# Kernel optimization log

Hardware: AMD Instinct MI355X
Metric: run time of the kernel (lower is better)

Reference implementation:

```python
import math
import jax, jax.numpy as jnp
import numpy as np

N = 2048          # batch size
D = 256           # embedding_dim
MEM = 16384       # memory_size
ANOMALY_WEIGHT = 1.0
TEMP = 0.1
MOMENTUM = 0.01
NCLS = 2          # binary phishing labels -> max(labels.max()+1, 2) == 2


def setup_inputs() -> dict:
    key = jax.random.key(0)
    ks = jax.random.split(key, 10)
    s = 1.0 / math.sqrt(D)  # nn.Linear default init range
    return {
        'z': jax.random.normal(ks[0], (N, D), jnp.float32),
        'labels': jax.random.randint(ks[1], (N,), 0, NCLS),
        'memory': jax.random.normal(ks[2], (MEM, D), jnp.float32),
        'memory_weights': jax.random.uniform(ks[3], (MEM,), jnp.float32),
        'running_mean': jnp.zeros((D,), jnp.float32),
        'running_cov': jnp.eye(D, dtype=jnp.float32),
        'Wq': jax.random.uniform(ks[4], (D, D), jnp.float32, -s, s),
        'bq': jax.random.uniform(ks[5], (D,), jnp.float32, -s, s),
        'Wk': jax.random.uniform(ks[6], (D, D), jnp.float32, -s, s),
        'bk': jax.random.uniform(ks[7], (D,), jnp.float32, -s, s),
        'Wv': jax.random.uniform(ks[8], (D, D), jnp.float32, -s, s),
        'bv': jax.random.uniform(ks[9], (D,), jnp.float32, -s, s),
    }


def reference(z, labels, memory, memory_weights, running_mean, running_cov,
              Wq, bq, Wk, bk, Wv, bv):
    # ---- update(z.detach(), labels): entire update path is detached in torch ----
    z_sg = jax.lax.stop_gradient(z)

    # _update_stats: EMA of batch mean / covariance (done before importance)
    mu = z_sg.mean(axis=0)                                  # [D]
    zc = z_sg - mu
    cov = zc.T @ zc / max(N - 1, 1)                         # [D, D]
    rm = (1.0 - MOMENTUM) * running_mean + MOMENTUM * mu
    rc = (1.0 - MOMENTUM) * running_cov + MOMENTUM * cov

    # _mahalanobis with updated running stats
    c = z_sg - rm
    cov_inv = jnp.linalg.inv(rc + 1e-6 * jnp.eye(D, dtype=rc.dtype))
    dist = jnp.sqrt(jnp.clip(jnp.einsum('nd,de,ne->n', c, cov_inv, c), 1e-8))
    a_norm = (dist - dist.min()) / (dist.max() - dist.min() + 1e-8)

    # _mi_proxy: KL(batch label dist || uniform), broadcast to all items
    counts = jnp.zeros((NCLS,), z.dtype).at[labels].add(1.0)
    p = counts / jnp.clip(counts.sum(), 1.0)
    # p / uniform == p * NCLS; clip inside log for safety (both classes present)
    kl = jnp.clip((p * jnp.log(jnp.clip(p * NCLS, 1e-8))).sum(), 0.0)
    importance = (1.0 + ANOMALY_WEIGHT * a_norm) * kl       # [N]

    # serial top-1 priority-queue eviction, in descending-importance order
    order = jnp.argsort(-importance)
    z_ord = z_sg[order]
    imp_ord = importance[order]

    def evict_step(state, inp):
        mem, w = state
        zi, imp = inp
        j = jnp.argmin(w)                   # weakest memory slot
        rep = imp > w[j]
        mem = mem.at[j].set(jnp.where(rep, zi, mem[j]))
        w = w.at[j].set(jnp.where(rep, imp, w[j]))
        return (mem, w), None

    (mem, _), _ = jax.lax.scan(evict_step, (memory, memory_weights), (z_ord, imp_ord))

    # ---- query(z): cross-attention over the (full) updated memory ----
    Q = z @ Wq.T + bq                       # [N, D]
    K = mem @ Wk.T + bk                     # [MEM, D]
    V = mem @ Wv.T + bv                     # [MEM, D]
    sc = (Q @ K.T) / math.sqrt(D)           # [N, MEM]
    attn = jax.nn.softmax(sc / TEMP, axis=-1)
    return z + 0.5 * (attn @ V)
```

## Files before the change

### kernel.cpp

```cpp
#include <hip/hip_runtime.h>
#include <math.h>

#define NB   2048
#define DE   256
#define MEMN 16384
#define CAND_CAP 256
#define FSPL 16
#define FKPS 1024
#define FIT  32

typedef __attribute__((ext_vector_type(8)))  short  short8;
typedef __attribute__((ext_vector_type(16))) float  float16;

static const size_t OFF_QB   = 0;
static const size_t OFF_KB   = 262144;
static const size_t OFF_VTB  = 2359296;
static const size_t OFF_LP   = 4456448;
static const size_t OFF_OPB  = 4521984;
static const size_t SO_A    = 0;
static const size_t SO_X    = 65536;
static const size_t SO_MUP  = 131072;
static const size_t SO_DIST = 147456;

__device__ inline unsigned short f2bf(float f) {
  unsigned u = __float_as_uint(f);
  unsigned r = (u + 0x7fffu + ((u >> 16) & 1u)) >> 16;
  return (unsigned short)r;
}
__device__ inline float bf2f(unsigned short s) {
  return __uint_as_float((unsigned)s << 16);
}

__device__ inline void bitonic_sort_u64(unsigned long long* key, int n, int tid, int nth) {
  for (int k = 2; k <= n; k <<= 1) {
    for (int j = k >> 1; j > 0; j >>= 1) {
      __syncthreads();
      for (int i = tid; i < n; i += nth) {
        int ixj = i ^ j;
        if (ixj > i) {
          unsigned long long a = key[i], b = key[ixj];
          bool up = ((i & k) == 0);
          if ((a > b) == up) { key[i] = b; key[ixj] = a; }
        }
      }
    }
  }
  __syncthreads();
}

__global__ __launch_bounds__(256) void mupart_kernel(const float* __restrict__ z,
                                                     float* __restrict__ mup,
                                                     float* __restrict__ Az) {
  int d = threadIdx.x;
  int r0 = blockIdx.x * 32;
  float4 zero4 = {0.f, 0.f, 0.f, 0.f};
  *(float4*)&Az[(size_t)blockIdx.x * 1024 + threadIdx.x * 4] = zero4;
  float s = 0.f;
  for (int r = 0; r < 32; ++r) s += z[(size_t)(r0 + r) * DE + d];
  mup[blockIdx.x * DE + d] = s;
}

__global__ __launch_bounds__(256) void covpart_kernel(const float* __restrict__ z,
                                                      float* __restrict__ A) {
  __shared__ float As[16][68];
  __shared__ float Bs[16][68];
  int tid = threadIdx.x, tx = tid & 15, ty = tid >> 4;
  int i0 = blockIdx.x * 64, j0 = blockIdx.y * 64;
  int nbase = blockIdx.z * 128;
  float acc[4][4] = {};
  for (int nt = 0; nt < 8; ++nt) {
    int n0 = nbase + nt * 16;
    for (int e = tid; e < 1024; e += 256) {
      int c = e & 63, nn = e >> 6;
      As[nn][c] = z[(size_t)(n0 + nn) * DE + i0 + c];
      Bs[nn][c] = z[(size_t)(n0 + nn) * DE + j0 + c];
    }
    __syncthreads();
#pragma unroll
    for (int nn = 0; nn < 16; ++nn) {
      float4 a4 = *(const float4*)&As[nn][ty * 4];
      float4 b4 = *(const float4*)&Bs[nn][tx * 4];
      acc[0][0] += a4.x*b4.x; acc[0][1] += a4.x*b4.y; acc[0][2] += a4.x*b4.z; acc[0][3] += a4.x*b4.w;
      acc[1][0] += a4.y*b4.x; acc[1][1] += a4.y*b4.y; acc[1][2] += a4.y*b4.z; acc[1][3] += a4.y*b4.w;
      acc[2][0] += a4.z*b4.x; acc[2][1] += a4.z*b4.y; acc[2][2] += a4.z*b4.z; acc[2][3] += a4.z*b4.w;
      acc[3][0] += a4.w*b4.x; acc[3][1] += a4.w*b4.y; acc[3][2] += a4.w*b4.z; acc[3][3] += a4.w*b4.w;
    }
    __syncthreads();
  }
  for (int r = 0; r < 4; ++r) {
    int i = i0 + ty * 4 + r;
    for (int c = 0; c < 4; ++c) {
      int j = j0 + tx * 4 + c;
      atomicAdd(&A[(size_t)i * DE + j], acc[r][c]);
    }
  }
}

__global__ __launch_bounds__(256) void gemmx_kernel(const float* __restrict__ ZtZ,
                                                    const float* __restrict__ rcov,
                                                    const float* __restrict__ mup,
                                                    float* __restrict__ X) {
  __shared__ float Ea[16][17];
  __shared__ float Eb[16][17];
  __shared__ float mus[256];
  int t = threadIdx.x, tx = t & 15, ty = t >> 4;
  int i0 = blockIdx.x * 16, j0 = blockIdx.y * 16;
  {
    float s = 0.f;
    for (int b = 0; b < 64; ++b) s += mup[b * DE + t];
    mus[t] = s;
  }
  __syncthreads();
  const float c1 = 0.01f / (float)(NB - 1);
  const float invN = 1.0f / (float)NB;
  float acc = 0.f;
  for (int k0 = 0; k0 < 256; k0 += 16) {
    int c = k0 + tx;
    {
      int r = i0 + ty;
      float base = 0.99f * rcov[(size_t)r * DE + c] +
                   c1 * (ZtZ[(size_t)r * DE + c] - mus[r] * mus[c] * invN);
      float e = -base;
      if (r == c) e += 1.0f - 1e-6f;
      Ea[ty][tx] = e;
    }
    {
      int r = j0 + ty;
      float base = 0.99f * rcov[(size_t)r * DE + c] +
                   c1 * (ZtZ[(size_t)r * DE + c] - mus[r] * mus[c] * invN);
      float e = -base;
      if (r == c) e += 1.0f - 1e-6f;
      Eb[ty][tx] = e;
    }
    __syncthreads();
#pragma unroll
    for (int k = 0; k < 16; ++k) acc += Ea[ty][k] * Eb[tx][k];
    __syncthreads();
  }
  int r = i0 + ty, c = j0 + tx;
  float base = 0.99f * rcov[(size_t)r * DE + c] +
               c1 * (ZtZ[(size_t)r * DE + c] - mus[r] * mus[c] * invN);
  float e = -base;
  if (r == c) e += 1.0f - 1e-6f;
  X[(size_t)r * DE + c] = acc + e + ((r == c) ? 1.0f : 0.0f);
}

__global__ __launch_bounds__(256) void dist_kernel(const float* __restrict__ z,
                                                   const float* __restrict__ rmean,
                                                   const float* __restrict__ mup,
                                                   const float* __restrict__ X,
                                                   float* __restrict__ dist) {
  __shared__ float cc[4][256];
  __shared__ float4 red[256];
  int n0 = blockIdx.x * 4, i = threadIdx.x;
  float s = 0.f;
  for (int b = 0; b < 64; ++b) s += mup[b * DE + i];
  float rmi = 0.99f * rmean[i] + 0.01f * s * (1.0f / (float)NB);
#pragma unroll
  for (int r = 0; r < 4; ++r) cc[r][i] = z[(size_t)(n0 + r) * DE + i] - rmi;
  __syncthreads();
  float y0 = 0.f, y1 = 0.f, y2 = 0.f, y3 = 0.f;
#pragma unroll 8
  for (int j = 0; j < DE; ++j) {
    float x = X[(size_t)j * DE + i];
    y0 += x * cc[0][j]; y1 += x * cc[1][j]; y2 += x * cc[2][j]; y3 += x * cc[3][j];
  }
  float4 v;
  v.x = y0 * cc[0][i]; v.y = y1 * cc[1][i]; v.z = y2 * cc[2][i]; v.w = y3 * cc[3][i];
  red[i] = v;
  __syncthreads();
  for (int sH = 128; sH > 0; sH >>= 1) {
    if (i < sH) {
      float4 a = red[i], b = red[i + sH];
      a.x += b.x; a.y += b.y; a.z += b.z; a.w += b.w;
      red[i] = a;
    }
    __syncthreads();
  }
  if (i < 4) {
    float4 tt = red[0];
    float d = (i == 0) ? tt.x : (i == 1) ? tt.y : (i == 2) ? tt.z : tt.w;
    dist[n0 + i] = sqrtf(fmaxf(d, 1e-8f));
  }
}

__global__ __launch_bounds__(1024) void update_kernel(const float* __restrict__ dist,
                                                      const int* __restrict__ labels,
                                                      const float* __restrict__ weights,
                                                      const float* __restrict__ z,
                                                      float* __restrict__ memory) {
  __shared__ unsigned long long ikeys[NB];
  __shared__ unsigned long long ck[CAND_CAP];
  __shared__ unsigned long long mred[1024];
  __shared__ int slots[CAND_CAP], srcs[CAND_CAP];
  __shared__ float smin[1024], smax[1024];
  __shared__ int scnt[1024];
  __shared__ float s_kl, s_dmin, s_inv;
  __shared__ int s_ccnt, s_m, s_stop;
  int t = threadIdx.x;

  float mn = 1e30f, mx = -1e30f; int c1 = 0;
  for (int n = t; n < NB; n += 1024) {
    float d = dist[n];
    mn = fminf(mn, d); mx = fmaxf(mx, d);
    c1 += labels[n];
  }
  smin[t] = mn; smax[t] = mx; scnt[t] = c1;
  __syncthreads();
  for (int s = 512; s > 0; s >>= 1) {
    if (t < s) {
      smin[t] = fminf(smin[t], smin[t + s]);
      smax[t] = fmaxf(smax[t], smax[t + s]);
      scnt[t] += scnt[t + s];
    }
    __syncthreads();
  }
  if (t == 0) {
    float p1 = (float)scnt[0] / (float)NB;
    float p0 = (float)(NB - scnt[0]) / (float)NB;
    float kl = p0 * logf(fmaxf(2.f * p0, 1e-8f)) + p1 * logf(fmaxf(2.f * p1, 1e-8f));
    s_kl = fmaxf(kl, 0.f);
    s_dmin = smin[0];
    s_inv = 1.0f / (smax[0] - smin[0] + 1e-8f);
    s_ccnt = 0; s_m = 0; s_stop = 0;
  }
  __syncthreads();
  float kl = s_kl;

  for (int n = t; n < NB; n += 1024) {
    float imp = (1.0f + (dist[n] - s_dmin) * s_inv) * kl;
    ikeys[n] = ((unsigned long long)(unsigned)(~__float_as_uint(imp)) << 32) | (unsigned)n;
  }
  float thresh = 2.f * kl;
  for (int j = t; j < MEMN; j += 1024) {
    float wv = weights[j];
    if (wv < thresh) {
      int p = atomicAdd(&s_ccnt, 1);
      if (p < CAND_CAP) ck[p] = ((unsigned long long)__float_as_uint(wv) << 32) | (unsigned)j;
    }
  }
  __syncthreads();
  int C = s_ccnt; if (C > CAND_CAP) C = CAND_CAP;
  for (int i = t; i < CAND_CAP; i += 1024)
    if (i >= C) ck[i] = 0xFFFFFFFFFFFFFFFFULL;
  bitonic_sort_u64(ck, CAND_CAP, t, 1024);

  float prevv = 0.f;
  for (int i = 0; i < C; ++i) {
    unsigned long long mymin = ikeys[t] < ikeys[t + 1024] ? ikeys[t] : ikeys[t + 1024];
    mred[t] = mymin;
    __syncthreads();
    for (int s = 512; s > 0; s >>= 1) {
      if (t < s) { if (mred[t + s] < mred[t]) mred[t] = mred[t + s]; }
      __syncthreads();
    }
    if (t == 0) {
      unsigned long long best = mred[0];
      float im = __uint_as_float(~(unsigned)(best >> 32));
      float wv = __uint_as_float((unsigned)(ck[i] >> 32));
      bool ok = (im > wv) && (i == 0 || prevv >= wv);
      if (ok) {
        slots[s_m] = (int)(ck[i] & 0xffffffffULL);
        srcs[s_m]  = (int)(best & 0xffffffffULL);
        s_m++;
        prevv = im;
        ikeys[(int)(best & 0xffffffffULL)] = ~0ULL;
      } else {
        s_stop = 1;
      }
    }
    __syncthreads();
    if (s_stop) break;
  }
  int m = s_m;
  for (int e = t; e < m * DE; e += 1024) {
    int i = e >> 8, d = e & 255;
    memory[(size_t)slots[i] * DE + d] = z[(size_t)srcs[i] * DE + d];
  }
}

__global__ __launch_bounds__(256, 1) void qkv_kernel(
    const float* __restrict__ z, const float* __restrict__ memory,
    const float* __restrict__ Wq, const float* __restrict__ bq,
    const float* __restrict__ Wk, const float* __restrict__ bk,
    const float* __restrict__ Wv, const float* __restrict__ bv,
    unsigned short* __restrict__ Qbf, unsigned short* __restrict__ Kbf,
    unsigned short* __restrict__ Vtb) {
  __shared__ unsigned short Bsh[64 * 264];
  int flat = blockIdx.x;
  const float *Af, *Bf, *bias;
  unsigned short* C;
  int bias_row, vtile, gx, gy, ldC;
  if (flat < 64) {
    gx = flat & 15; gy = flat >> 4;
    Af = z; Bf = Wq; bias = bq; bias_row = 0; vtile = 0; C = Qbf; ldC = DE;
  } else if (flat < 576) {
    int f = flat - 64; gx = f & 127; gy = f >> 7;
    Af = memory; Bf = Wk; bias = bk; bias_row = 0; vtile = 0; C = Kbf; ldC = DE;
  } else {
    int f = flat - 576; gx = f & 1; gy = f >> 1;
    Af = Wv; Bf = memory; bias = bv; bias_row = 1; vtile = 1; C = Vtb; ldC = 0;
  }

  int tid = threadIdx.x;
  int w = tid >> 6, lane = tid & 63;
  int m = lane & 31, h = lane >> 5;
  int arow = gx * 128 + w * 32 + m;
  int n0 = gy * 64;

  short8 af[16];
#pragma unroll
  for (int kc = 0; kc < 16; ++kc) {
    const float* src = &Af[(size_t)arow * DE + kc * 16 + h * 8];
    float4 f0 = *(const float4*)&src[0];
    float4 f1 = *(const float4*)&src[4];
    short8 v;
    v[0] = (short)f2bf(f0.x); v[1] = (short)f2bf(f0.y);
    v[2] = (short)f2bf(f0.z); v[3] = (short)f2bf(f0.w);
    v[4] = (short)f2bf(f1.x); v[5] = (short)f2bf(f1.y);
    v[6] = (short)f2bf(f1.z); v[7] = (short)f2bf(f1.w);
    af[kc] = v;
  }
  {
    int r = tid >> 2, q = tid & 3;
    const float* src = &Bf[(size_t)(n0 + r) * DE + q * 64];
    unsigned short* dst = &Bsh[r * 264 + q * 64];
#pragma unroll
    for (int j = 0; j < 8; ++j) {
      float4 f0 = *(const float4*)&src[j * 8];
      float4 f1 = *(const float4*)&src[j * 8 + 4];
      short8 v;
      v[0] = (short)f2bf(f0.x); v[1] = (short)f2bf(f0.y);
      v[2] = (short)f2bf(f0.z); v[3] = (short)f2bf(f0.w);
      v[4] = (short)f2bf(f1.x); v[5] = (short)f2bf(f1.y);
      v[6] = (short)f2bf(f1.z); v[7] = (short)f2bf(f1.w);
      *(short8*)&dst[j * 8] = v;
    }
  }
  __syncthreads();

  float16 a0 = {}, a1 = {};
#pragma unroll
  for (int kc = 0; kc < 16; ++kc) {
    short8 b0 = *(const short8*)&Bsh[(0 * 32 + m) * 264 + kc * 16 + h * 8];
    short8 b1 = *(const short8*)&Bsh[(1 * 32 + m) * 264 + kc * 16 + h * 8];
    a0 = __builtin_amdgcn_mfma_f32_32x32x16_bf16(af[kc], b0, a0, 0, 0, 0);
    a1 = __builtin_amdgcn_mfma_f32_32x32x16_bf16(af[kc], b1, a1, 0, 0, 0);
  }
#pragma unroll
  for (int r = 0; r < 16; ++r) {
    int rr = (r & 3) + 8 * (r >> 2) + 4 * h;
    int orow = gx * 128 + w * 32 + rr;
    int oc0 = n0 + m, oc1 = n0 + 32 + m;
    float bb0 = bias_row ? bias[orow] : bias[oc0];
    float bb1 = bias_row ? bias[orow] : bias[oc1];
    if (!vtile) {
      C[(size_t)orow * ldC + oc0] = f2bf(a0[r] + bb0);
      C[(size_t)orow * ldC + oc1] = f2bf(a1[r] + bb1);
    } else {
      C[(size_t)(oc0 >> 5) * 8192 + (size_t)orow * 32 + (oc0 & 31)] = f2bf(a0[r] + bb0);
      C[(size_t)(oc1 >> 5) * 8192 + (size_t)orow * 32 + (oc1 & 31)] = f2bf(a1[r] + bb1);
    }
  }
}

__global__ __launch_bounds__(256, 2) void flash_kernel(
    const unsigned short* __restrict__ Qb, const unsigned short* __restrict__ Kb,
    const unsigned short* __restrict__ Vtb, unsigned short* __restrict__ Opb,
    float* __restrict__ Lp) {
  __shared__ unsigned short Ks[32 * 264];
  __shared__ unsigned short Vs[128 * 40];
  __shared__ unsigned short Ps[4][32 * 40];

  int tid = threadIdx.x;
  int w = tid >> 6, lane = tid & 63;
  int m = lane & 31, h = lane >> 5;
  int sp = blockIdx.x, qg = blockIdx.y, dh = blockIdx.z;
  int myrow = qg * 128 + w * 32 + m;

  short8 qf[16];
#pragma unroll
  for (int kc = 0; kc < 16; ++kc)
    qf[kc] = *(const short8*)&Qb[(size_t)myrow * DE + kc * 16 + h * 8];
  short8 ones;
#pragma unroll
  for (int j = 0; j < 8; ++j) ones[j] = (short)0x3F80;

  float16 O[4] = {};
  float16 l = {};

  short8 kreg[4], vreg[2];
  {
    int kb = sp * FKPS;
#pragma unroll
    for (int i = 0; i < 4; ++i) {
      int c = i * 256 + tid, kr = c >> 5, kc = c & 31;
      kreg[i] = *(const short8*)&Kb[(size_t)(kb + kr) * DE + kc * 8];
    }
    const unsigned short* vg = &Vtb[(size_t)(kb >> 5) * 8192 + (size_t)dh * 4096];
#pragma unroll
    for (int i = 0; i < 2; ++i) {
      int c = i * 256 + tid;
      vreg[i] = *(const short8*)&vg[c * 8];
    }
  }

  for (int it = 0; it < FIT; ++it) {
    __syncthreads();
#pragma unroll
    for (int i = 0; i < 4; ++i) {
      int c = i * 256 + tid, kr = c >> 5, kc = c & 31;
      *(short8*)&Ks[kr * 264 + kc * 8] = kreg[i];
    }
#pragma unroll
    for (int i = 0; i < 2; ++i) {
      int c = i * 256 + tid, dr = c >> 2, dc = c & 3;
      *(short8*)&Vs[dr * 40 + dc * 8] = vreg[i];
    }
    if (it + 1 < FIT) {
      int kb = sp * FKPS + (it + 1) * 32;
#pragma unroll
      for (int i = 0; i < 4; ++i) {
        int c = i * 256 + tid, kr = c >> 5, kc = c & 31;
        kreg[i] = *(const short8*)&Kb[(size_t)(kb + kr) * DE + kc * 8];
      }
      const unsigned short* vg = &Vtb[(size_t)(kb >> 5) * 8192 + (size_t)dh * 4096];
#pragma unroll
      for (int i = 0; i < 2; ++i) {
        int c = i * 256 + tid;
        vreg[i] = *(const short8*)&vg[c * 8];
      }
    }
    __syncthreads();

    float16 s0 = {}, s1 = {};
    __builtin_amdgcn_s_setprio(1);
#pragma unroll
    for (int kc = 0; kc < 16; kc += 2) {
      short8 b0 = *(const short8*)&Ks[m * 264 + kc * 16 + h * 8];
      short8 b1 = *(const short8*)&Ks[m * 264 + (kc + 1) * 16 + h * 8];
      s0 = __builtin_amdgcn_mfma_f32_32x32x16_bf16(qf[kc], b0, s0, 0, 0, 0);
      s1 = __builtin_amdgcn_mfma_f32_32x32x16_bf16(qf[kc + 1], b1, s1, 0, 0, 0);
    }
    __builtin_amdgcn_s_setprio(0);
#pragma unroll
    for (int r = 0; r < 16; ++r) {
      int row = (r & 3) + 8 * (r >> 2) + 4 * h;
      Ps[w][row * 40 + m] = f2bf(__expf(fmaf(s0[r] + s1[r], 0.625f, -11.0903549f)));
    }
    short8 pa0 = *(const short8*)&Ps[w][m * 40 + h * 8];
    short8 pa1 = *(const short8*)&Ps[w][m * 40 + 16 + h * 8];
    __builtin_amdgcn_s_setprio(1);
    l = __builtin_amdgcn_mfma_f32_32x32x16_bf16(pa0, ones, l, 0, 0, 0);
    l = __builtin_amdgcn_mfma_f32_32x32x16_bf16(pa1, ones, l, 0, 0, 0);
#pragma unroll
    for (int ct = 0; ct < 4; ++ct) {
      short8 vb0 = *(const short8*)&Vs[(ct * 32 + m) * 40 + h * 8];
      short8 vb1 = *(const short8*)&Vs[(ct * 32 + m) * 40 + 16 + h * 8];
      O[ct] = __builtin_amdgcn_mfma_f32_32x32x16_bf16(pa0, vb0, O[ct], 0, 0, 0);
      O[ct] = __builtin_amdgcn_mfma_f32_32x32x16_bf16(pa1, vb1, O[ct], 0, 0, 0);
    }
    __builtin_amdgcn_s_setprio(0);
  }

  size_t ob = ((size_t)sp * NB + qg * 128 + w * 32) * DE + dh * 128;
#pragma unroll
  for (int ct = 0; ct < 4; ++ct)
#pragma unroll
    for (int r = 0; r < 16; ++r) {
      int rr = (r & 3) + 8 * (r >> 2) + 4 * h;
      Opb[ob + (size_t)rr * DE + ct * 32 + m] = f2bf(O[ct][r]);
    }
  if (dh == 0 && m == 0) {
#pragma unroll
    for (int r = 0; r < 16; ++r) {
      int rr = (r & 3) + 8 * (r >> 2) + 4 * h;
      Lp[sp * NB + qg * 128 + w * 32 + rr] = l[r];
    }
  }
}

__global__ __launch_bounds__(256) void combine_kernel(const float* __restrict__ z,
                                                      const unsigned short* __restrict__ Opb,
                                                      const float* __restrict__ Lp,
                                                      float* __restrict__ out) {
  int n = blockIdx.x, c = threadIdx.x;
  float num = 0.f, den = 0.f;
#pragma unroll
  for (int s = 0; s < FSPL; ++s) {
    den += Lp[s * NB + n];
    num += bf2f(Opb[((size_t)s * NB + n) * DE + c]);
  }
  size_t base = (size_t)n * DE + c;
  out[base] = z[base] + 0.5f * num / den;
}

extern "C" void kernel_launch(void* const* d_in, const int* in_sizes, int n_in,
                              void* d_out, int out_size, void* d_ws, size_t ws_size,
                              hipStream_t stream) {
  (void)in_sizes; (void)n_in; (void)out_size; (void)ws_size;
  const float* z       = (const float*)d_in[0];
  const int*   labels  = (const int*)d_in[1];
  float*       memory  = (float*)d_in[2];
  const float* weights = (const float*)d_in[3];
  const float* rmean   = (const float*)d_in[4];
  const float* rcov    = (const float*)d_in[5];
  const float* Wq      = (const float*)d_in[6];
  const float* bq      = (const float*)d_in[7];
  const float* Wk      = (const float*)d_in[8];
  const float* bk      = (const float*)d_in[9];
  const float* Wv      = (const float*)d_in[10];
  const float* bv      = (const float*)d_in[11];
  float* out = (float*)d_out;
  float* ws  = (float*)d_ws;

  unsigned short* Qbf = (unsigned short*)(ws + OFF_QB);
  unsigned short* Kbf = (unsigned short*)(ws + OFF_KB);
  unsigned short* Vtb = (unsigned short*)(ws + OFF_VTB);
  float* Lp           = ws + OFF_LP;
  unsigned short* Opb = (unsigned short*)(ws + OFF_OPB);
  float* SB    = ws + OFF_OPB;
  float* A     = SB + SO_A;
  float* X     = SB + SO_X;
  float* mup   = SB + SO_MUP;
  float* dist  = SB + SO_DIST;

  mupart_kernel<<<64, 256, 0, stream>>>(z, mup, A);
  covpart_kernel<<<dim3(4, 4, 16), 256, 0, stream>>>(z, A);
  gemmx_kernel<<<dim3(16, 16), 256, 0, stream>>>(A, rcov, mup, X);
  dist_kernel<<<NB / 4, 256, 0, stream>>>(z, rmean, mup, X, dist);
  update_kernel<<<1, 1024, 0, stream>>>(dist, labels, weights, z, memory);
  qkv_kernel<<<1088, 256, 0, stream>>>(z, memory, Wq, bq, Wk, bk, Wv, bv, Qbf, Kbf, Vtb);
  flash_kernel<<<dim3(FSPL, NB / 128, 2), 256, 0, stream>>>(Qbf, Kbf, Vtb, Opb, Lp);
  combine_kernel<<<NB, 256, 0, stream>>>(z, Opb, Lp, out);
}
```

Baseline: 259.1 us.

## Double-buffer K/V LDS tiles in flash kernel with one barrier per iteration

The flash attention loop now keeps two LDS buffers for the K and V tiles. It stores the next tile into the alternate buffer while computing on the current one, which cuts the two barriers per iteration down to one and overlaps the LDS writes with the MFMA work. The exponential is also rewritten as exp2f with pre-scaled constants. The cost is doubled LDS use for K and V, which could lower occupancy, and a slightly different rounding of the softmax numerator.

```diff
diff --git a/kernel.cpp b/kernel.cpp
--- a/kernel.cpp
+++ b/kernel.cpp
@@ -368,8 +368,8 @@
     const unsigned short* __restrict__ Qb, const unsigned short* __restrict__ Kb,
     const unsigned short* __restrict__ Vtb, unsigned short* __restrict__ Opb,
     float* __restrict__ Lp) {
-  __shared__ unsigned short Ks[32 * 264];
-  __shared__ unsigned short Vs[128 * 40];
+  __shared__ unsigned short Ks[2][32 * 264];
+  __shared__ unsigned short Vs[2][128 * 40];
   __shared__ unsigned short Ps[4][32 * 40];
 
   int tid = threadIdx.x;
@@ -389,56 +389,53 @@
   float16 O[4] = {};
   float16 l = {};
 
+  int kc_r = tid >> 5, kc_c = tid & 31;
+  int vd_r = tid >> 2, vd_c = tid & 3;
+
   short8 kreg[4], vreg[2];
-  {
-    int kb = sp * FKPS;
-#pragma unroll
-    for (int i = 0; i < 4; ++i) {
-      int c = i * 256 + tid, kr = c >> 5, kc = c & 31;
-      kreg[i] = *(const short8*)&Kb[(size_t)(kb + kr) * DE + kc * 8];
-    }
-    const unsigned short* vg = &Vtb[(size_t)(kb >> 5) * 8192 + (size_t)dh * 4096];
-#pragma unroll
-    for (int i = 0; i < 2; ++i) {
-      int c = i * 256 + tid;
-      vreg[i] = *(const short8*)&vg[c * 8];
-    }
-  }
+#define LOAD_TILE(kb_)                                                          \
+  {                                                                             \
+    int kb = (kb_);                                                             \
+    _Pragma("unroll")                                                           \
+    for (int i = 0; i < 4; ++i) {                                               \
+      int c = i * 256 + tid, kr = c >> 5, kcol = c & 31;                        \
+      kreg[i] = *(const short8*)&Kb[(size_t)(kb + kr) * DE + kcol * 8];         \
+    }                                                                           \
+    const unsigned short* vg = &Vtb[(size_t)((kb) >> 5) * 8192 + (size_t)dh * 4096]; \
+    _Pragma("unroll")                                                           \
+    for (int i = 0; i < 2; ++i) {                                               \
+      int c = i * 256 + tid;                                                    \
+      vreg[i] = *(const short8*)&vg[c * 8];                                     \
+    }                                                                           \
+  }
+#define STORE_TILE(buf)                                                         \
+  {                                                                             \
+    _Pragma("unroll")                                                           \
+    for (int i = 0; i < 4; ++i)                                                 \
+      *(short8*)&Ks[buf][(kc_r + i * 8) * 264 + kc_c * 8] = kreg[i];            \
+    _Pragma("unroll")                                                           \
+    for (int i = 0; i < 2; ++i)                                                 \
+      *(short8*)&Vs[buf][(vd_r + i * 64) * 40 + vd_c * 8] = vreg[i];            \
+  }
+
+  LOAD_TILE(sp * FKPS);
+  STORE_TILE(0);
+  LOAD_TILE(sp * FKPS + 32);
+  __syncthreads();
 
   for (int it = 0; it < FIT; ++it) {
-    __syncthreads();
-#pragma unroll
-    for (int i = 0; i < 4; ++i) {
-      int c = i * 256 + tid, kr = c >> 5, kc = c & 31;
-      *(short8*)&Ks[kr * 264 + kc * 8] = kreg[i];
-    }
-#pragma unroll
-    for (int i = 0; i < 2; ++i) {
-      int c = i * 256 + tid, dr = c >> 2, dc = c & 3;
-      *(short8*)&Vs[dr * 40 + dc * 8] = vreg[i];
-    }
+    int cur = it & 1;
     if (it + 1 < FIT) {
-      int kb = sp * FKPS + (it + 1) * 32;
-#pragma unroll
-      for (int i = 0; i < 4; ++i) {
-        int c = i * 256 + tid, kr = c >> 5, kc = c & 31;
-        kreg[i] = *(const short8*)&Kb[(size_t)(kb + kr) * DE + kc * 8];
-      }
-      const unsigned short* vg = &Vtb[(size_t)(kb >> 5) * 8192 + (size_t)dh * 4096];
-#pragma unroll
-      for (int i = 0; i < 2; ++i) {
-        int c = i * 256 + tid;
-        vreg[i] = *(const short8*)&vg[c * 8];
-      }
-    }
-    __syncthreads();
+      STORE_TILE(cur ^ 1);
+      if (it + 2 < FIT) LOAD_TILE(sp * FKPS + (it + 2) * 32);
+    }
 
     float16 s0 = {}, s1 = {};
     __builtin_amdgcn_s_setprio(1);
 #pragma unroll
     for (int kc = 0; kc < 16; kc += 2) {
-      short8 b0 = *(const short8*)&Ks[m * 264 + kc * 16 + h * 8];
-      short8 b1 = *(const short8*)&Ks[m * 264 + (kc + 1) * 16 + h * 8];
+      short8 b0 = *(const short8*)&Ks[cur][m * 264 + kc * 16 + h * 8];
+      short8 b1 = *(const short8*)&Ks[cur][m * 264 + (kc + 1) * 16 + h * 8];
       s0 = __builtin_amdgcn_mfma_f32_32x32x16_bf16(qf[kc], b0, s0, 0, 0, 0);
       s1 = __builtin_amdgcn_mfma_f32_32x32x16_bf16(qf[kc + 1], b1, s1, 0, 0, 0);
     }
@@ -446,7 +443,7 @@
 #pragma unroll
     for (int r = 0; r < 16; ++r) {
       int row = (r & 3) + 8 * (r >> 2) + 4 * h;
-      Ps[w][row * 40 + m] = f2bf(__expf(fmaf(s0[r] + s1[r], 0.625f, -11.0903549f)));
+      Ps[w][row * 40 + m] = f2bf(exp2f(fmaf(s0[r] + s1[r], 0.90168440f, -16.0f)));
     }
     short8 pa0 = *(const short8*)&Ps[w][m * 40 + h * 8];
     short8 pa1 = *(const short8*)&Ps[w][m * 40 + 16 + h * 8];
@@ -455,13 +452,16 @@
     l = __builtin_amdgcn_mfma_f32_32x32x16_bf16(pa1, ones, l, 0, 0, 0);
 #pragma unroll
     for (int ct = 0; ct < 4; ++ct) {
-      short8 vb0 = *(const short8*)&Vs[(ct * 32 + m) * 40 + h * 8];
-      short8 vb1 = *(const short8*)&Vs[(ct * 32 + m) * 40 + 16 + h * 8];
+      short8 vb0 = *(const short8*)&Vs[cur][(ct * 32 + m) * 40 + h * 8];
+      short8 vb1 = *(const short8*)&Vs[cur][(ct * 32 + m) * 40 + 16 + h * 8];
       O[ct] = __builtin_amdgcn_mfma_f32_32x32x16_bf16(pa0, vb0, O[ct], 0, 0, 0);
       O[ct] = __builtin_amdgcn_mfma_f32_32x32x16_bf16(pa1, vb1, O[ct], 0, 0, 0);
     }
     __builtin_amdgcn_s_setprio(0);
-  }
+    __syncthreads();
+  }
+#undef LOAD_TILE
+#undef STORE_TILE
 
   size_t ob = ((size_t)sp * NB + qg * 128 + w * 32) * DE + dh * 128;
 #pragma unroll
```

Measured after the change: 263.2 us. No clear change (+1.6%).

## Keep softmax probabilities in registers via transposed QK MFMA and lane swaps

Applied to the files above, without the earlier changes.

Swaps the MFMA operands so the score tile comes out transposed, letting each lane hold one query row's probabilities. These are packed to bf16 with v_cvt_pk_bf16_f32 and exchanged across half-waves with permlane32_swap, so they can feed the PV MFMA directly without the LDS staging buffer. The row sum is now accumulated in scalar registers instead of through an MFMA against a vector of ones, and the exponent uses exp2f with the scale folded into the constant. The point is to cut LDS writes, LDS reads, a barrier-like dependency and two MFMAs per iteration. The cost is more VALU work and reliance on the lane layout being right.

```diff
diff --git a/kernel.cpp b/kernel.cpp
--- a/kernel.cpp
+++ b/kernel.cpp
@@ -11,6 +11,8 @@
 
 typedef __attribute__((ext_vector_type(8)))  short  short8;
 typedef __attribute__((ext_vector_type(16))) float  float16;
+typedef __attribute__((ext_vector_type(4)))  unsigned uint4v;
+typedef __attribute__((ext_vector_type(2)))  unsigned uint2v;
 
 static const size_t OFF_QB   = 0;
 static const size_t OFF_KB   = 262144;
@@ -29,6 +31,26 @@
 }
 __device__ inline float bf2f(unsigned short s) {
   return __uint_as_float((unsigned)s << 16);
+}
+
+__device__ inline unsigned cvtpk_bf16(float lo, float hi) {
+  unsigned r;
+  asm("v_cvt_pk_bf16_f32 %0, %1, %2" : "=v"(r) : "v"(lo), "v"(hi));
+  return r;
+}
+
+__device__ inline void halfswap(unsigned& lo, unsigned& hi, int h) {
+#if __has_builtin(__builtin_amdgcn_permlane32_swap)
+  (void)h;
+  uint2v r = __builtin_amdgcn_permlane32_swap(lo, hi, false, false);
+  lo = r.x; hi = r.y;
+#else
+  unsigned a = (unsigned)__shfl_xor((int)lo, 32, 64);
+  unsigned b = (unsigned)__shfl_xor((int)hi, 32, 64);
+  unsigned nlo = (h == 0) ? lo : b;
+  unsigned nhi = (h == 0) ? a  : hi;
+  lo = nlo; hi = nhi;
+#endif
 }
 
 __device__ inline void bitonic_sort_u64(unsigned long long* key, int n, int tid, int nth) {
@@ -370,7 +392,6 @@
     float* __restrict__ Lp) {
   __shared__ unsigned short Ks[32 * 264];
   __shared__ unsigned short Vs[128 * 40];
-  __shared__ unsigned short Ps[4][32 * 40];
 
   int tid = threadIdx.x;
   int w = tid >> 6, lane = tid & 63;
@@ -382,12 +403,9 @@
 #pragma unroll
   for (int kc = 0; kc < 16; ++kc)
     qf[kc] = *(const short8*)&Qb[(size_t)myrow * DE + kc * 16 + h * 8];
-  short8 ones;
-#pragma unroll
-  for (int j = 0; j < 8; ++j) ones[j] = (short)0x3F80;
 
   float16 O[4] = {};
-  float16 l = {};
+  float lacc = 0.f;
 
   short8 kreg[4], vreg[2];
   {
@@ -439,20 +457,37 @@
     for (int kc = 0; kc < 16; kc += 2) {
       short8 b0 = *(const short8*)&Ks[m * 264 + kc * 16 + h * 8];
       short8 b1 = *(const short8*)&Ks[m * 264 + (kc + 1) * 16 + h * 8];
-      s0 = __builtin_amdgcn_mfma_f32_32x32x16_bf16(qf[kc], b0, s0, 0, 0, 0);
-      s1 = __builtin_amdgcn_mfma_f32_32x32x16_bf16(qf[kc + 1], b1, s1, 0, 0, 0);
+      s0 = __builtin_amdgcn_mfma_f32_32x32x16_bf16(b0, qf[kc], s0, 0, 0, 0);
+      s1 = __builtin_amdgcn_mfma_f32_32x32x16_bf16(b1, qf[kc + 1], s1, 0, 0, 0);
     }
     __builtin_amdgcn_s_setprio(0);
-#pragma unroll
-    for (int r = 0; r < 16; ++r) {
-      int row = (r & 3) + 8 * (r >> 2) + 4 * h;
-      Ps[w][row * 40 + m] = f2bf(__expf(fmaf(s0[r] + s1[r], 0.625f, -11.0903549f)));
-    }
-    short8 pa0 = *(const short8*)&Ps[w][m * 40 + h * 8];
-    short8 pa1 = *(const short8*)&Ps[w][m * 40 + 16 + h * 8];
+
+    float p[16];
+#pragma unroll
+    for (int r = 0; r < 16; ++r)
+      p[r] = exp2f(fmaf(s0[r] + s1[r], 0.90168440f, -16.0f));
+
+    lacc += ((p[0] + p[1]) + (p[2] + p[3])) + ((p[4] + p[5]) + (p[6] + p[7])) +
+            ((p[8] + p[9]) + (p[10] + p[11])) + ((p[12] + p[13]) + (p[14] + p[15]));
+
+    unsigned c0 = cvtpk_bf16(p[0],  p[1]);
+    unsigned c1 = cvtpk_bf16(p[2],  p[3]);
+    unsigned c2 = cvtpk_bf16(p[4],  p[5]);
+    unsigned c3 = cvtpk_bf16(p[6],  p[7]);
+    unsigned c4 = cvtpk_bf16(p[8],  p[9]);
+    unsigned c5 = cvtpk_bf16(p[10], p[11]);
+    unsigned c6 = cvtpk_bf16(p[12], p[13]);
+    unsigned c7 = cvtpk_bf16(p[14], p[15]);
+    halfswap(c0, c2, h);
+    halfswap(c1, c3, h);
+    halfswap(c4, c6, h);
+    halfswap(c5, c7, h);
+    uint4v w0v = {c0, c1, c2, c3};
+    uint4v w1v = {c4, c5, c6, c7};
+    short8 pa0 = __builtin_bit_cast(short8, w0v);
+    short8 pa1 = __builtin_bit_cast(short8, w1v);
+
     __builtin_amdgcn_s_setprio(1);
-    l = __builtin_amdgcn_mfma_f32_32x32x16_bf16(pa0, ones, l, 0, 0, 0);
-    l = __builtin_amdgcn_mfma_f32_32x32x16_bf16(pa1, ones, l, 0, 0, 0);
 #pragma unroll
     for (int ct = 0; ct < 4; ++ct) {
       short8 vb0 = *(const short8*)&Vs[(ct * 32 + m) * 40 + h * 8];
@@ -471,13 +506,9 @@
       int rr = (r & 3) + 8 * (r >> 2) + 4 * h;
       Opb[ob + (size_t)rr * DE + ct * 32 + m] = f2bf(O[ct][r]);
     }
-  if (dh == 0 && m == 0) {
-#pragma unroll
-    for (int r = 0; r < 16; ++r) {
-      int rr = (r & 3) + 8 * (r >> 2) + 4 * h;
-      Lp[sp * NB + qg * 128 + w * 32 + rr] = l[r];
-    }
-  }
+  float ltot = lacc + __shfl_xor(lacc, 32, 64);
+  if (dh == 0 && h == 0)
+    Lp[sp * NB + qg * 128 + w * 32 + m] = ltot;
 }
 
 __global__ __launch_bounds__(256) void combine_kernel(const float* __restrict__ z,
```

Result: no change. 260.0 us (+0.4%).
